# Kernel optimization log

Measured on AMD Instinct MI355X. Metric: run time of the kernel, lower is better.

The kernel has to match this reference:

```python
import jax, jax.numpy as jnp
import numpy as np

N_NODES = 50000
N_EDGES = 600000
D_FEAT = 128
NHID = 128
N_CLASSES = 40


def gcn_conv(x, W, b, src, dst, n_nodes):
    """PyG-style GCNConv: out = D^{-1/2} (A + I) D^{-1/2} (x W) + b.

    src/dst: [E'] edge endpoints including self-loops; messages are gathered
    from src and scatter-added at dst with symmetric normalization.
    """
    h = x @ W  # [N, out] -- transform before propagate (linearity => same math)
    deg = jax.ops.segment_sum(jnp.ones_like(dst, dtype=h.dtype), dst,
                              num_segments=n_nodes)  # in-degree incl. self-loop
    dinv = jnp.where(deg > 0, jax.lax.rsqrt(deg), 0.0)
    norm = dinv[src] * dinv[dst]  # [E']
    msg = h[src] * norm[:, None]  # [E', out] gather + scale
    out = jax.ops.segment_sum(msg, dst, num_segments=n_nodes)  # scatter-add
    return out + b


def setup_inputs() -> dict:
    key = jax.random.key(0)
    ks = jax.random.split(key, 8)
    x = jax.random.normal(ks[0], (N_NODES, D_FEAT), dtype=jnp.float32)
    edge_index = jax.random.randint(ks[1], (2, N_EDGES), 0, N_NODES, dtype=jnp.int64)
    # Glorot-ish scaled params
    W1 = jax.random.normal(ks[2], (D_FEAT, NHID), dtype=jnp.float32) / np.sqrt(D_FEAT)
    b1 = jnp.zeros((NHID,), dtype=jnp.float32)
    W2 = jax.random.normal(ks[3], (NHID, NHID), dtype=jnp.float32) / np.sqrt(NHID)
    b2 = jnp.zeros((NHID,), dtype=jnp.float32)
    Wlin = jax.random.normal(ks[4], (NHID, N_CLASSES), dtype=jnp.float32) / np.sqrt(NHID)
    blin = jnp.zeros((N_CLASSES,), dtype=jnp.float32)
    return {"x": x, "edge_index": edge_index, "W1": W1, "b1": b1,
            "W2": W2, "b2": b2, "Wlin": Wlin, "blin": blin}


def reference(x, edge_index, W1, b1, W2, b2, Wlin, blin):
    n = x.shape[0]
    loop = jnp.arange(n, dtype=edge_index.dtype)
    src = jnp.concatenate([edge_index[0], loop])  # add self-loops
    dst = jnp.concatenate([edge_index[1], loop])
    h = gcn_conv(x, W1, b1, src, dst, n)
    h = jnp.tanh(h)  # dropout is identity in eval mode
    h = gcn_conv(h, W2, b2, src, dst, n)
    h = jnp.tanh(h)
    return h @ Wlin + blin  # [N, num_classes]
```

## Files before the change

### kernel.cpp

```cpp
#include <hip/hip_runtime.h>
#include <cmath>

#define D 128
#define NCLS 40
#define GG 391
#define CAP 64

typedef __bf16 bfrag __attribute__((ext_vector_type(8)));
typedef float ffrag __attribute__((ext_vector_type(4)));
typedef unsigned int u32;
typedef unsigned int u32x4 __attribute__((ext_vector_type(4)));

__device__ inline float fast_tanh(float x) {
  float ax = __builtin_fabsf(x);
  float z = __expf(-2.0f * ax);
  float r = (1.0f - z) * __builtin_amdgcn_rcpf(1.0f + z);
  return copysignf(r, x);
}

__global__ __launch_bounds__(256) void prep(const float* __restrict__ W1, const float* __restrict__ W2,
                                            const float* __restrict__ Wl, __bf16* __restrict__ Wt1,
                                            __bf16* __restrict__ Wt2, __bf16* __restrict__ Wlt,
                                            int* __restrict__ deg, int N, int nb) {
  const int b = blockIdx.x;
  const int tid = threadIdx.x;
  if (b < nb) {
    int i = b * 256 + tid;
    if (i < N) deg[i] = 0;
    return;
  }
  if (b < nb + 64) {
    int j = (b - nb) * 256 + tid;
    Wt1[j] = (__bf16)W1[(j & 127) * D + (j >> 7)];
    return;
  }
  int j = (b - nb - 64) * 256 + tid;
  if (j < 16384) {
    Wt2[j] = (__bf16)W2[(j & 127) * D + (j >> 7)];
  } else if (j < 16384 + 48 * D) {
    int q = j - 16384;
    int n = q >> 7, k = q & 127;
    Wlt[q] = (n < NCLS) ? (__bf16)Wl[k * NCLS + n] : (__bf16)0.0f;
  }
}

__global__ __launch_bounds__(256) void mega1(const float* __restrict__ A, const __bf16* __restrict__ Wt1,
                                             __bf16* __restrict__ C, int N,
                                             const int* __restrict__ src, const int* __restrict__ dst, int E,
                                             int* __restrict__ deg, int* __restrict__ csr) {
  const int b = blockIdx.x;
  const int tid = threadIdx.x;
  if (b >= GG) {
    int e = (b - GG) * 256 + tid;
    if (e < E) {
      int s = src[e], d = dst[e];
      int pos = atomicAdd(&deg[d], 1);
      if (pos < CAP) csr[d * CAP + pos] = s;
    }
    return;
  }
  __shared__ __align__(16) __bf16 Bs[128][136];
  const int wave = tid >> 6, lane = tid & 63;
  const int row0 = b * 128 + wave * 32;
  const int koff = (lane >> 4) * 8;

  for (int i = tid; i < 128 * 16; i += 256) {
    int n = i >> 4, seg = i & 15;
    *(uint4*)&Bs[n][seg * 8] = *(const uint4*)(Wt1 + n * D + seg * 8);
  }

  bfrag a[2][4];
#pragma unroll
  for (int mt = 0; mt < 2; ++mt) {
    int r = row0 + mt * 16 + (lane & 15);
    int rc = r < N ? r : N - 1;
    const float* p = A + (size_t)rc * D;
#pragma unroll
    for (int kk = 0; kk < 4; ++kk) {
      float4 u = *(const float4*)(p + kk * 32 + koff);
      float4 v = *(const float4*)(p + kk * 32 + koff + 4);
      bfrag f;
      f[0] = (__bf16)u.x; f[1] = (__bf16)u.y; f[2] = (__bf16)u.z; f[3] = (__bf16)u.w;
      f[4] = (__bf16)v.x; f[5] = (__bf16)v.y; f[6] = (__bf16)v.z; f[7] = (__bf16)v.w;
      a[mt][kk] = f;
    }
  }
  __syncthreads();

  ffrag acc[2][8];
#pragma unroll
  for (int mt = 0; mt < 2; ++mt)
#pragma unroll
    for (int n = 0; n < 8; ++n) acc[mt][n] = (ffrag){0.f, 0.f, 0.f, 0.f};

#pragma unroll
  for (int kk = 0; kk < 4; ++kk) {
#pragma unroll
    for (int n = 0; n < 8; ++n) {
      bfrag bb = *(const bfrag*)(&Bs[n * 16 + (lane & 15)][kk * 32 + koff]);
      acc[0][n] = __builtin_amdgcn_mfma_f32_16x16x32_bf16(a[0][kk], bb, acc[0][n], 0, 0, 0);
      acc[1][n] = __builtin_amdgcn_mfma_f32_16x16x32_bf16(a[1][kk], bb, acc[1][n], 0, 0, 0);
    }
  }

  int ocol = lane & 15;
#pragma unroll
  for (int mt = 0; mt < 2; ++mt) {
    int orow0 = row0 + mt * 16 + (lane >> 4) * 4;
#pragma unroll
    for (int n = 0; n < 8; ++n)
#pragma unroll
      for (int i = 0; i < 4; ++i) {
        int r = orow0 + i;
        if (r < N) C[(size_t)r * D + n * 16 + ocol] = (__bf16)acc[mt][n][i];
      }
  }
}

__global__ __launch_bounds__(256) void scale_rows(__bf16* __restrict__ t, const int* __restrict__ deg, int N) {
  int i = blockIdx.x * 256 + threadIdx.x;
  int row = i >> 4;
  if (row >= N) return;
  float dv = rsqrtf((float)deg[row] + 1.0f);
  __bf16* p = t + (size_t)row * D + (i & 15) * 8;
  bfrag v = *(const bfrag*)p;
  bfrag o;
#pragma unroll
  for (int k = 0; k < 8; ++k) o[k] = (__bf16)(dv * (float)v[k]);
  *(bfrag*)p = o;
}

__device__ inline void gather16s(const __bf16* __restrict__ t, const int* __restrict__ deg,
                                 const int* __restrict__ csr, const float* __restrict__ bias,
                                 __bf16 (*Hs)[136], float* dvs, int node0, int wave, int lane, int N) {
  const int g = lane >> 4, sl = lane & 15;
  const int node = node0 + wave * 4 + g;
  const int nd = node < N ? node : N - 1;

  int esr = csr[nd * CAP + sl];
  const int cnt = deg[nd];
  bfrag tv = *(const bfrag*)(t + (size_t)nd * D + sl * 8);

  const int jm = cnt < CAP ? cnt : CAP;
  const float dv = rsqrtf((float)cnt + 1.0f);
  if (sl == 0) dvs[wave * 4 + g] = dv;

  int mx = jm;
  int o1 = __shfl_xor(mx, 16, 64);
  mx = mx > o1 ? mx : o1;
  int o2 = __shfl_xor(mx, 32, 64);
  mx = mx > o2 ? mx : o2;
  const int jmw = __builtin_amdgcn_readfirstlane(mx);

  float acc[8];
#pragma unroll
  for (int i = 0; i < 8; ++i) acc[i] = (float)tv[i];

  for (int base = 0; base < jmw; base += 16) {
    if (base > 0) esr = csr[nd * CAP + base + sl];
    int es = ((unsigned)esr < (unsigned)N) ? esr : nd;
    int nin = jmw - base; nin = nin < 16 ? nin : 16;
    for (int j = 0; j < nin; ++j) {
      int s = __shfl(es, g * 16 + j, 64);
      bfrag r = *(const bfrag*)(t + (size_t)s * D + sl * 8);
      if (base + j < jm) {
#pragma unroll
        for (int i = 0; i < 8; ++i) acc[i] += (float)r[i];
      }
    }
  }

  float4 b0 = *(const float4*)(bias + sl * 8);
  float4 b1 = *(const float4*)(bias + sl * 8 + 4);
  bfrag o;
  o[0] = (__bf16)fast_tanh(dv * acc[0] + b0.x);
  o[1] = (__bf16)fast_tanh(dv * acc[1] + b0.y);
  o[2] = (__bf16)fast_tanh(dv * acc[2] + b0.z);
  o[3] = (__bf16)fast_tanh(dv * acc[3] + b0.w);
  o[4] = (__bf16)fast_tanh(dv * acc[4] + b1.x);
  o[5] = (__bf16)fast_tanh(dv * acc[5] + b1.y);
  o[6] = (__bf16)fast_tanh(dv * acc[6] + b1.z);
  o[7] = (__bf16)fast_tanh(dv * acc[7] + b1.w);
  *(u32x4*)&Hs[wave * 4 + g][sl * 8] = *(u32x4*)&o;
}

__global__ __launch_bounds__(256) void gather_gemm(const __bf16* __restrict__ t, const int* __restrict__ deg,
                                                   const int* __restrict__ csr, const float* __restrict__ bias,
                                                   const __bf16* __restrict__ Wt, __bf16* __restrict__ C, int N) {
  __shared__ __align__(16) __bf16 Hs[32][136];
  __shared__ float dvs[32];
  const int tid = threadIdx.x;
  const int wave = tid >> 6, lane = tid & 63;
  const int g = lane >> 4, sl = lane & 15;
  const int node0 = blockIdx.x * 32;

  gather16s(t, deg, csr, bias, Hs, dvs, node0, wave, lane, N);
  gather16s(t, deg, csr, bias, Hs + 16, dvs + 16, node0 + 16, wave, lane, N);
  __syncthreads();

  const int koff = g * 8;
#pragma unroll
  for (int rt = 0; rt < 2; ++rt) {
    bfrag a[4];
#pragma unroll
    for (int kk = 0; kk < 4; ++kk) a[kk] = *(const bfrag*)(&Hs[rt * 16 + sl][kk * 32 + koff]);
    ffrag acc2[2];
    acc2[0] = (ffrag){0.f, 0.f, 0.f, 0.f};
    acc2[1] = (ffrag){0.f, 0.f, 0.f, 0.f};
#pragma unroll
    for (int nt = 0; nt < 2; ++nt) {
      const __bf16* wp = Wt + (size_t)(wave * 32 + nt * 16 + sl) * D;
      bfrag bfr[4];
#pragma unroll
      for (int kk = 0; kk < 4; ++kk) bfr[kk] = *(const bfrag*)(wp + kk * 32 + koff);
#pragma unroll
      for (int kk = 0; kk < 4; ++kk)
        acc2[nt] = __builtin_amdgcn_mfma_f32_16x16x32_bf16(a[kk], bfr[kk], acc2[nt], 0, 0, 0);
    }
#pragma unroll
    for (int nt = 0; nt < 2; ++nt) {
      int ccol = wave * 32 + nt * 16 + sl;
#pragma unroll
      for (int i = 0; i < 4; ++i) {
        int r = node0 + rt * 16 + g * 4 + i;
        if (r < N) C[(size_t)r * D + ccol] = (__bf16)(dvs[rt * 16 + g * 4 + i] * acc2[nt][i]);
      }
    }
  }
}

__global__ __launch_bounds__(256) void gather_head(const __bf16* __restrict__ t, const int* __restrict__ deg,
                                                   const int* __restrict__ csr, const float* __restrict__ bias,
                                                   const __bf16* __restrict__ Wlt, const float* __restrict__ blin,
                                                   float* __restrict__ out, int N) {
  __shared__ __align__(16) __bf16 Hs[32][136];
  __shared__ float dvs[32];
  const int tid = threadIdx.x;
  const int wave = tid >> 6, lane = tid & 63;
  const int g = lane >> 4, sl = lane & 15;
  const int node0 = blockIdx.x * 32;

  gather16s(t, deg, csr, bias, Hs, dvs, node0, wave, lane, N);
  gather16s(t, deg, csr, bias, Hs + 16, dvs + 16, node0 + 16, wave, lane, N);
  __syncthreads();

  if (wave < 3) {
    const int koff = g * 8;
#pragma unroll
    for (int rt = 0; rt < 2; ++rt) {
      bfrag a[4];
#pragma unroll
      for (int kk = 0; kk < 4; ++kk) a[kk] = *(const bfrag*)(&Hs[rt * 16 + sl][kk * 32 + koff]);
      ffrag acc2 = (ffrag){0.f, 0.f, 0.f, 0.f};
      const __bf16* wp = Wlt + (size_t)(wave * 16 + sl) * D;
      bfrag bfr[4];
#pragma unroll
      for (int kk = 0; kk < 4; ++kk) bfr[kk] = *(const bfrag*)(wp + kk * 32 + koff);
#pragma unroll
      for (int kk = 0; kk < 4; ++kk)
        acc2 = __builtin_amdgcn_mfma_f32_16x16x32_bf16(a[kk], bfr[kk], acc2, 0, 0, 0);

      int ccol = wave * 16 + sl;
      if (ccol < NCLS) {
        float bl = blin[ccol];
#pragma unroll
        for (int i = 0; i < 4; ++i) {
          int r = node0 + rt * 16 + g * 4 + i;
          if (r < N) out[(size_t)r * NCLS + ccol] = acc2[i] + bl;
        }
      }
    }
  }
}

extern "C" void kernel_launch(void* const* d_in, const int* in_sizes, int n_in,
                              void* d_out, int out_size, void* d_ws, size_t ws_size,
                              hipStream_t stream) {
  const float* x    = (const float*)d_in[0];
  const int*   ei   = (const int*)d_in[1];
  const float* W1   = (const float*)d_in[2];
  const float* b1   = (const float*)d_in[3];
  const float* W2   = (const float*)d_in[4];
  const float* b2   = (const float*)d_in[5];
  const float* Wlin = (const float*)d_in[6];
  const float* blin = (const float*)d_in[7];
  float* out = (float*)d_out;

  const int N = in_sizes[0] / D;
  const int E = in_sizes[1] / 2;
  const int* srcp = ei;
  const int* dstp = ei + E;

  char* ws = (char*)d_ws;
  int*    deg = (int*)ws;
  __bf16* Wt2 = (__bf16*)(ws + ((size_t)512 << 10));
  __bf16* Wlt = (__bf16*)(ws + ((size_t)560 << 10));
  __bf16* Wt1 = (__bf16*)(ws + ((size_t)608 << 10));
  int*    csr = (int*)(ws + ((size_t)1 << 20));
  __bf16* tb  = (__bf16*)(ws + ((size_t)16 << 20));
  __bf16* hb  = (__bf16*)(ws + ((size_t)32 << 20));

  const int nb = (N + 255) / 256;
  const int eb = (E + 255) / 256;
  const int cvb = (16384 + 48 * D + 255) / 256;
  const int gb = (N + 31) / 32;
  dim3 b256(256);

  prep<<<nb + 64 + cvb, b256, 0, stream>>>(W1, W2, Wlin, Wt1, Wt2, Wlt, deg, N, nb);
  mega1<<<GG + eb, b256, 0, stream>>>(x, Wt1, tb, N, srcp, dstp, E, deg, csr);
  scale_rows<<<(N * 16 + 255) / 256, b256, 0, stream>>>(tb, deg, N);
  gather_gemm<<<gb, b256, 0, stream>>>(tb, deg, csr, b1, Wt2, hb, N);
  gather_head<<<gb, b256, 0, stream>>>(hb, deg, csr, b2, Wlt, blin, out, N);
}
```

Before: 182.2 us.

## Shrink first-layer GEMM tile to 16 rows per block and guard CSR loads

The first-layer x@W1 GEMM in mega1 now uses 16-row blocks with each wave computing a 32-column slice, reading W1 fragments straight from global memory instead of staging the full weight in LDS. This launches many more small blocks (N/16 instead of 391), which raises parallelism and drops the LDS fill and barrier. The cost is that every block re-reads W1 from cache. Separately, the gather loop loads CSR entries only for valid slots (sl < remaining), which avoids reading uninitialised entries and removes the up-front prefetch.

```diff
diff --git a/kernel.cpp b/kernel.cpp
--- a/kernel.cpp
+++ b/kernel.cpp
@@ -3,7 +3,6 @@
 
 #define D 128
 #define NCLS 40
-#define GG 391
 #define CAP 64
 
 typedef __bf16 bfrag __attribute__((ext_vector_type(8)));
@@ -47,11 +46,11 @@
 __global__ __launch_bounds__(256) void mega1(const float* __restrict__ A, const __bf16* __restrict__ Wt1,
                                              __bf16* __restrict__ C, int N,
                                              const int* __restrict__ src, const int* __restrict__ dst, int E,
-                                             int* __restrict__ deg, int* __restrict__ csr) {
+                                             int* __restrict__ deg, int* __restrict__ csr, int GB1) {
   const int b = blockIdx.x;
   const int tid = threadIdx.x;
-  if (b >= GG) {
-    int e = (b - GG) * 256 + tid;
+  if (b >= GB1) {
+    int e = (b - GB1) * 256 + tid;
     if (e < E) {
       int s = src[e], d = dst[e];
       int pos = atomicAdd(&deg[d], 1);
@@ -59,61 +58,46 @@
     }
     return;
   }
-  __shared__ __align__(16) __bf16 Bs[128][136];
   const int wave = tid >> 6, lane = tid & 63;
-  const int row0 = b * 128 + wave * 32;
-  const int koff = (lane >> 4) * 8;
-
-  for (int i = tid; i < 128 * 16; i += 256) {
-    int n = i >> 4, seg = i & 15;
-    *(uint4*)&Bs[n][seg * 8] = *(const uint4*)(Wt1 + n * D + seg * 8);
-  }
-
-  bfrag a[2][4];
-#pragma unroll
-  for (int mt = 0; mt < 2; ++mt) {
-    int r = row0 + mt * 16 + (lane & 15);
-    int rc = r < N ? r : N - 1;
-    const float* p = A + (size_t)rc * D;
-#pragma unroll
-    for (int kk = 0; kk < 4; ++kk) {
-      float4 u = *(const float4*)(p + kk * 32 + koff);
-      float4 v = *(const float4*)(p + kk * 32 + koff + 4);
-      bfrag f;
-      f[0] = (__bf16)u.x; f[1] = (__bf16)u.y; f[2] = (__bf16)u.z; f[3] = (__bf16)u.w;
-      f[4] = (__bf16)v.x; f[5] = (__bf16)v.y; f[6] = (__bf16)v.z; f[7] = (__bf16)v.w;
-      a[mt][kk] = f;
-    }
-  }
-  __syncthreads();
-
-  ffrag acc[2][8];
-#pragma unroll
-  for (int mt = 0; mt < 2; ++mt)
-#pragma unroll
-    for (int n = 0; n < 8; ++n) acc[mt][n] = (ffrag){0.f, 0.f, 0.f, 0.f};
-
+  const int g = lane >> 4, sl = lane & 15;
+  const int row0 = b * 16;
+  const int koff = g * 8;
+
+  int r = row0 + sl;
+  int rc = r < N ? r : N - 1;
+  const float* p = A + (size_t)rc * D;
+  bfrag a[4];
 #pragma unroll
   for (int kk = 0; kk < 4; ++kk) {
-#pragma unroll
-    for (int n = 0; n < 8; ++n) {
-      bfrag bb = *(const bfrag*)(&Bs[n * 16 + (lane & 15)][kk * 32 + koff]);
-      acc[0][n] = __builtin_amdgcn_mfma_f32_16x16x32_bf16(a[0][kk], bb, acc[0][n], 0, 0, 0);
-      acc[1][n] = __builtin_amdgcn_mfma_f32_16x16x32_bf16(a[1][kk], bb, acc[1][n], 0, 0, 0);
-    }
-  }
-
-  int ocol = lane & 15;
-#pragma unroll
-  for (int mt = 0; mt < 2; ++mt) {
-    int orow0 = row0 + mt * 16 + (lane >> 4) * 4;
-#pragma unroll
-    for (int n = 0; n < 8; ++n)
-#pragma unroll
-      for (int i = 0; i < 4; ++i) {
-        int r = orow0 + i;
-        if (r < N) C[(size_t)r * D + n * 16 + ocol] = (__bf16)acc[mt][n][i];
-      }
+    float4 u = *(const float4*)(p + kk * 32 + koff);
+    float4 v = *(const float4*)(p + kk * 32 + koff + 4);
+    bfrag f;
+    f[0] = (__bf16)u.x; f[1] = (__bf16)u.y; f[2] = (__bf16)u.z; f[3] = (__bf16)u.w;
+    f[4] = (__bf16)v.x; f[5] = (__bf16)v.y; f[6] = (__bf16)v.z; f[7] = (__bf16)v.w;
+    a[kk] = f;
+  }
+
+  ffrag acc2[2];
+  acc2[0] = (ffrag){0.f, 0.f, 0.f, 0.f};
+  acc2[1] = (ffrag){0.f, 0.f, 0.f, 0.f};
+#pragma unroll
+  for (int nt = 0; nt < 2; ++nt) {
+    const __bf16* wp = Wt1 + (size_t)(wave * 32 + nt * 16 + sl) * D;
+    bfrag bfr[4];
+#pragma unroll
+    for (int kk = 0; kk < 4; ++kk) bfr[kk] = *(const bfrag*)(wp + kk * 32 + koff);
+#pragma unroll
+    for (int kk = 0; kk < 4; ++kk)
+      acc2[nt] = __builtin_amdgcn_mfma_f32_16x16x32_bf16(a[kk], bfr[kk], acc2[nt], 0, 0, 0);
+  }
+#pragma unroll
+  for (int nt = 0; nt < 2; ++nt) {
+    int ccol = wave * 32 + nt * 16 + sl;
+#pragma unroll
+    for (int i = 0; i < 4; ++i) {
+      int rr = row0 + g * 4 + i;
+      if (rr < N) C[(size_t)rr * D + ccol] = (__bf16)acc2[nt][i];
+    }
   }
 }
 
@@ -136,11 +120,7 @@
   const int g = lane >> 4, sl = lane & 15;
   const int node = node0 + wave * 4 + g;
   const int nd = node < N ? node : N - 1;
-
-  int esr = csr[nd * CAP + sl];
   const int cnt = deg[nd];
-  bfrag tv = *(const bfrag*)(t + (size_t)nd * D + sl * 8);
-
   const int jm = cnt < CAP ? cnt : CAP;
   const float dv = rsqrtf((float)cnt + 1.0f);
   if (sl == 0) dvs[wave * 4 + g] = dv;
@@ -152,13 +132,15 @@
   mx = mx > o2 ? mx : o2;
   const int jmw = __builtin_amdgcn_readfirstlane(mx);
 
+  bfrag tv = *(const bfrag*)(t + (size_t)nd * D + sl * 8);
   float acc[8];
 #pragma unroll
   for (int i = 0; i < 8; ++i) acc[i] = (float)tv[i];
 
   for (int base = 0; base < jmw; base += 16) {
-    if (base > 0) esr = csr[nd * CAP + base + sl];
-    int es = ((unsigned)esr < (unsigned)N) ? esr : nd;
+    int rem = jm - base;
+    int es = nd;
+    if (sl < rem) es = csr[nd * CAP + base + sl];
     int nin = jmw - base; nin = nin < 16 ? nin : 16;
     for (int j = 0; j < nin; ++j) {
       int s = __shfl(es, g * 16 + j, 64);
@@ -303,11 +285,12 @@
   const int nb = (N + 255) / 256;
   const int eb = (E + 255) / 256;
   const int cvb = (16384 + 48 * D + 255) / 256;
+  const int gb1 = (N + 15) / 16;
   const int gb = (N + 31) / 32;
   dim3 b256(256);
 
   prep<<<nb + 64 + cvb, b256, 0, stream>>>(W1, W2, Wlin, Wt1, Wt2, Wlt, deg, N, nb);
-  mega1<<<GG + eb, b256, 0, stream>>>(x, Wt1, tb, N, srcp, dstp, E, deg, csr);
+  mega1<<<gb1 + eb, b256, 0, stream>>>(x, Wt1, tb, N, srcp, dstp, E, deg, csr, gb1);
   scale_rows<<<(N * 16 + 255) / 256, b256, 0, stream>>>(tb, deg, N);
   gather_gemm<<<gb, b256, 0, stream>>>(tb, deg, csr, b1, Wt2, hb, N);
   gather_head<<<gb, b256, 0, stream>>>(hb, deg, csr, b2, Wlt, blin, out, N);
```

Result: slower. 209.3 us (+14.9%).
